# Kernel tuning notes

Measured on AMD Instinct MI355X. Metric: run time of the kernel, lower is better.

The kernel has to match this reference:

```python
import jax, jax.numpy as jnp
import numpy as np

THRESHOLD = 0.5
NEG_POS_RATIO = 3
ALPHA = 1.0


def cxcy_to_xy(c):
    return jnp.concatenate([c[..., :2] - c[..., 2:] / 2, c[..., :2] + c[..., 2:] / 2], axis=-1)


def xy_to_cxcy(x):
    return jnp.concatenate([(x[..., :2] + x[..., 2:]) / 2, x[..., 2:] - x[..., :2]], axis=-1)


def cxcy_to_gcxgcy(cxcy, priors_cxcy):
    return jnp.concatenate([
        (cxcy[..., :2] - priors_cxcy[..., :2]) / (priors_cxcy[..., 2:] / 10.0),
        jnp.log(cxcy[..., 2:] / priors_cxcy[..., 2:]) * 5.0,
    ], axis=-1)


def jaccard(a, b):
    # a: [M,4] xy, b: [P,4] xy -> IoU [M,P]
    lt = jnp.maximum(a[:, None, :2], b[None, :, :2])
    rb = jnp.minimum(a[:, None, 2:], b[None, :, 2:])
    wh = jnp.clip(rb - lt, 0.0)
    inter = wh[..., 0] * wh[..., 1]
    area_a = (a[:, 2] - a[:, 0]) * (a[:, 3] - a[:, 1])
    area_b = (b[:, 2] - b[:, 0]) * (b[:, 3] - b[:, 1])
    return inter / (area_a[:, None] + area_b[None, :] - inter)


def setup_inputs() -> dict:
    key = jax.random.key(0)
    k1, k2, k3, k4, k5, k6, k7 = jax.random.split(key, 7)
    B, P, C, M = 32, 8732, 81, 20
    predicted_locs = jax.random.normal(k1, (B, P, 4), dtype=jnp.float32)
    predicted_scores = jax.random.normal(k2, (B, P, C), dtype=jnp.float32)
    # priors in cxcy format, well inside the unit square
    p_cxy = jax.random.uniform(k3, (P, 2), minval=0.05, maxval=0.95)
    p_wh = jax.random.uniform(k4, (P, 2), minval=0.05, maxval=0.30)
    priors_cxcy = jnp.concatenate([p_cxy, p_wh], axis=-1).astype(jnp.float32)
    # GT boxes: random cxcy -> xy, clipped to [0,1]
    b_cxy = jax.random.uniform(k5, (B, M, 2), minval=0.1, maxval=0.9)
    b_wh = jax.random.uniform(k6, (B, M, 2), minval=0.05, maxval=0.40)
    boxes = jnp.clip(cxcy_to_xy(jnp.concatenate([b_cxy, b_wh], axis=-1)), 0.0, 1.0).astype(jnp.float32)
    labels = jax.random.randint(k7, (B, M), 1, C, dtype=jnp.int64 if jax.config.jax_enable_x64 else jnp.int32)
    return {
        "predicted_locs": predicted_locs,
        "predicted_scores": predicted_scores,
        "boxes": boxes,
        "labels": labels,
        "priors_cxcy": priors_cxcy,
    }


def _match_one(boxes_i, labels_i, priors_cxcy, priors_xy):
    M = boxes_i.shape[0]
    overlap = jaccard(boxes_i, priors_xy)                 # [M, P]
    ov_per_prior = overlap.max(axis=0)                    # [P]
    obj_per_prior = overlap.argmax(axis=0)                # [P]
    prior_per_obj = overlap.argmax(axis=1)                # [M]
    # force-assign each object to its best prior
    obj_per_prior = obj_per_prior.at[prior_per_obj].set(jnp.arange(M))
    ov_per_prior = ov_per_prior.at[prior_per_obj].set(1.0)
    lab = labels_i[obj_per_prior]                         # [P]
    lab = jnp.where(ov_per_prior < THRESHOLD, 0, lab)
    true_locs = cxcy_to_gcxgcy(xy_to_cxcy(boxes_i[obj_per_prior]), priors_cxcy)  # [P,4]
    return true_locs, lab


def reference(predicted_locs, predicted_scores, boxes, labels, priors_cxcy):
    priors_xy = cxcy_to_xy(priors_cxcy)
    true_locs, true_classes = jax.vmap(_match_one, in_axes=(0, 0, None, None))(
        boxes, labels, priors_cxcy, priors_xy)            # [B,P,4], [B,P]

    pos = true_classes > 0                                # [B,P]
    n_pos = pos.sum(axis=1)                               # [B]
    n_pos_total = n_pos.sum().astype(jnp.float32)

    # smooth L1 over positive priors (mean over all selected elements)
    d = predicted_locs - true_locs
    ad = jnp.abs(d)
    sl1 = jnp.where(ad < 1.0, 0.5 * d * d, ad - 0.5)      # [B,P,4]
    loc_loss = jnp.sum(sl1 * pos[..., None]) / (n_pos_total * 4.0)

    # per-prior cross entropy
    logp = jax.nn.log_softmax(predicted_scores, axis=-1)
    ce = -jnp.take_along_axis(logp, true_classes[..., None], axis=-1)[..., 0]  # [B,P]

    conf_pos = jnp.sum(jnp.where(pos, ce, 0.0))
    neg = jnp.where(pos, 0.0, ce)
    neg_sorted = -jnp.sort(-neg, axis=1)                  # descending per image
    ranks = jnp.arange(neg.shape[1])[None, :]
    hard = ranks < (NEG_POS_RATIO * n_pos)[:, None]
    conf_neg = jnp.sum(neg_sorted * hard)

    conf_loss = (conf_neg + conf_pos) / n_pos_total
    return conf_loss, ALPHA * loc_loss
```

## Files before the change

### kernel.cpp

```cpp
#include <hip/hip_runtime.h>
#include <math.h>

#define NB 32
#define NP 8732
#define NC 81
#define NM 20
#define CHUNKS 35
#define NROWS (NB * NP)
#define NGROUPS (NROWS / 4)
#define CE_BLOCKS ((NGROUPS + 63) / 64)
#define MT 1024
#define MV 9

typedef unsigned long long ull;
#define AGENT __HIP_MEMORY_SCOPE_AGENT


__global__ __launch_bounds__(256)
void match_force_kernel(const float* __restrict__ boxes,
                        const int*   __restrict__ labels,
                        const float* __restrict__ priors,
                        ull*      __restrict__ bestpart,
                        unsigned* __restrict__ labobj,
                        int*      __restrict__ chunkdone)
{
    const int b = blockIdx.x / CHUNKS;
    const int chunk = blockIdx.x % CHUNKS;
    const int tid = threadIdx.x;
    const int p = chunk * 256 + tid;
    const bool valid = p < NP;

    __shared__ float bxs[NM][4];
    __shared__ float areaA[NM];
    __shared__ int   labL[NM];
    __shared__ float iouT[256 * 21];
    __shared__ ull   wcand[4][NM];
    __shared__ int   flagLast;
    __shared__ int   pps[NM];

    if (tid < NM * 4) ((float*)bxs)[tid] = boxes[b * NM * 4 + tid];
    if (tid >= 128 && tid < 128 + NM) labL[tid - 128] = labels[b * NM + (tid - 128)];
    if (tid == 0) flagLast = 0;
    __syncthreads();
    if (tid < NM) areaA[tid] = (bxs[tid][2] - bxs[tid][0]) * (bxs[tid][3] - bxs[tid][1]);
    __syncthreads();

    float4 pc = reinterpret_cast<const float4*>(priors)[valid ? p : 0];
    const float px1 = pc.x - pc.z * 0.5f;
    const float py1 = pc.y - pc.w * 0.5f;
    const float px2 = pc.x + pc.z * 0.5f;
    const float py2 = pc.y + pc.w * 0.5f;
    const float pa  = (px2 - px1) * (py2 - py1);

    float bov = -1.f; int bm = 0;
    const int tbase = tid * 21;
#pragma unroll
    for (int m = 0; m < NM; m++) {
        float ix1 = fmaxf(bxs[m][0], px1);
        float iy1 = fmaxf(bxs[m][1], py1);
        float ix2 = fminf(bxs[m][2], px2);
        float iy2 = fminf(bxs[m][3], py2);
        float iw = fmaxf(ix2 - ix1, 0.f);
        float ih = fmaxf(iy2 - iy1, 0.f);
        float inter = iw * ih;
        float iou = inter / (areaA[m] + pa - inter);
        if (iou > bov) { bov = iou; bm = m; }
        iouT[tbase + m] = valid ? iou : -1.f;
    }
    if (valid) {
        int lab = (bov < 0.5f) ? 0 : labL[bm];
        __hip_atomic_store(&labobj[(size_t)b * NP + p],
                           (unsigned)lab | ((unsigned)bm << 8),
                           __ATOMIC_RELAXED, AGENT);
    }
    __syncthreads();

    const int lane = tid & 63, wid = tid >> 6;
    if (lane < NM) {
        const int m = lane;
        float bv = -1.f; int bt = 0;
        const int t0 = wid * 64;
        for (int t = t0; t < t0 + 64; t++) {
            float v = iouT[t * 21 + m];
            if (v > bv) { bv = v; bt = t; }
        }
        wcand[wid][m] = (bv < 0.f) ? 0ull
            : ((((ull)__float_as_uint(bv)) << 32) | (unsigned)~(unsigned)(chunk * 256 + bt));
    }
    __syncthreads();
    if (tid < NM) {
        ull k = wcand[0][tid];
        if (wcand[1][tid] > k) k = wcand[1][tid];
        if (wcand[2][tid] > k) k = wcand[2][tid];
        if (wcand[3][tid] > k) k = wcand[3][tid];
        __hip_atomic_store(&bestpart[(size_t)(b * CHUNKS + chunk) * NM + tid], k,
                           __ATOMIC_RELAXED, AGENT);
    }
    __syncthreads();
    if (tid == 0) {
        int old = __hip_atomic_fetch_add(&chunkdone[b], 1, __ATOMIC_ACQ_REL, AGENT);
        if (old == CHUNKS - 1) flagLast = 1;
    }
    __syncthreads();

    if (flagLast) {
        if (tid < NM) {
            ull k = 0ull;
            for (int c = 0; c < CHUNKS; c++) {
                ull v = __hip_atomic_load(&bestpart[(size_t)(b * CHUNKS + c) * NM + tid],
                                          __ATOMIC_RELAXED, AGENT);
                if (v > k) k = v;
            }
            pps[tid] = (int)~(unsigned)(k & 0xFFFFFFFFull);
        }
        __syncthreads();
        if (tid < NM) {
            int pp = pps[tid];
            bool win = true;
            for (int m2 = tid + 1; m2 < NM; m2++)
                if (pps[m2] == pp) win = false;
            if (win)
                __hip_atomic_store(&labobj[(size_t)b * NP + pp],
                                   (unsigned)labL[tid] | ((unsigned)tid << 8),
                                   __ATOMIC_RELAXED, AGENT);
        }
    }
}

__global__ __launch_bounds__(256)
void ce_kernel(const float* __restrict__ scores,
               const float* __restrict__ plocs,
               const float* __restrict__ boxes,
               const float* __restrict__ priors,
               const unsigned* __restrict__ labobj,
               float* __restrict__ neg,
               float* __restrict__ perimgPos,
               float* __restrict__ perimgLoc,
               int*   __restrict__ nposarr)
{
    __shared__ float bsum, blocsum;
    __shared__ int   bnp[2];
    const int tid = threadIdx.x;
    if (tid == 0) { bsum = 0.f; blocsum = 0.f; }
    if (tid < 2) bnp[tid] = 0;
    __syncthreads();

    const int q = tid & 3;
    const long long g = (long long)blockIdx.x * 64 + (tid >> 2);
    const bool gvalid = g < NGROUPS;
    const float4* gp = reinterpret_cast<const float4*>(scores) + (gvalid ? g : 0) * 81;

    float s0 = 0.f, s1 = 0.f, s2 = 0.f, s3 = 0.f;
#pragma unroll
    for (int j = 0; j < 20; j++) {
        float4 A = gp[q + 4 * j];
        float ex = __expf(A.x), ey = __expf(A.y), ez = __expf(A.z), ew = __expf(A.w);
        if (j <= 4) {
            s0 += (ex + ey) + (ez + ew);
        } else if (j >= 6 && j <= 9) {
            s1 += (ex + ey) + (ez + ew);
        } else if (j >= 11 && j <= 14) {
            s2 += (ex + ey) + (ez + ew);
        } else if (j >= 16) {
            s3 += (ex + ey) + (ez + ew);
        } else {
            const int bnd = (j == 5) ? 81 : (j == 10) ? 162 : 243;
            const int e0 = (q + 4 * j) * 4;
            float lo_ = ((e0     < bnd) ? ex : 0.f) + ((e0 + 1 < bnd) ? ey : 0.f)
                      + ((e0 + 2 < bnd) ? ez : 0.f) + ((e0 + 3 < bnd) ? ew : 0.f);
            float hi_ = ((e0     < bnd) ? 0.f : ex) + ((e0 + 1 < bnd) ? 0.f : ey)
                      + ((e0 + 2 < bnd) ? 0.f : ez) + ((e0 + 3 < bnd) ? 0.f : ew);
            if (j == 5)      { s0 += lo_; s1 += hi_; }
            else if (j == 10){ s1 += lo_; s2 += hi_; }
            else             { s2 += lo_; s3 += hi_; }
        }
    }
    if (q == 0) {
        float4 L = gp[80];
        s3 += (__expf(L.x) + __expf(L.y)) + (__expf(L.z) + __expf(L.w));
    }
    s0 += __shfl_xor(s0, 1);  s0 += __shfl_xor(s0, 2);
    s1 += __shfl_xor(s1, 1);  s1 += __shfl_xor(s1, 2);
    s2 += __shfl_xor(s2, 1);  s2 += __shfl_xor(s2, 2);
    s3 += __shfl_xor(s3, 1);  s3 += __shfl_xor(s3, 2);

    if (gvalid) {
        const float srow = (q == 0) ? s0 : (q == 1) ? s1 : (q == 2) ? s2 : s3;
        const long long r = g * 4 + q;
        const int b = (int)(r / NP);
        const int p = (int)(r - (long long)b * NP);
        const int bfirst = (int)(((long long)blockIdx.x * 256) / NP);
        const unsigned lo = labobj[r];
        const int lab = lo & 0xFF;
        const int obj = lo >> 8;
        float labval = scores[(size_t)r * NC + lab];
        float ce = __logf(srow) - labval;

        if (lab > 0) {
            neg[r] = 0.f;
            atomicAdd(&bsum, ce);
            atomicAdd(&bnp[b - bfirst], 1);
            float4 pcr = reinterpret_cast<const float4*>(priors)[p];
            const float* bx = boxes + ((size_t)b * NM + obj) * 4;
            float x1 = bx[0], y1 = bx[1], x2 = bx[2], y2 = bx[3];
            float bcx = (x1 + x2) * 0.5f, bcy = (y1 + y2) * 0.5f;
            float bw = x2 - x1, bh = y2 - y1;
            float g0 = (bcx - pcr.x) / (pcr.z / 10.f);
            float g1 = (bcy - pcr.y) / (pcr.w / 10.f);
            float g2 = __logf(bw / pcr.z) * 5.f;
            float g3 = __logf(bh / pcr.w) * 5.f;
            float4 pl = reinterpret_cast<const float4*>(plocs)[r];
            float t = 0.f, d, ad;
            d = pl.x - g0; ad = fabsf(d); t += (ad < 1.f) ? 0.5f * d * d : ad - 0.5f;
            d = pl.y - g1; ad = fabsf(d); t += (ad < 1.f) ? 0.5f * d * d : ad - 0.5f;
            d = pl.z - g2; ad = fabsf(d); t += (ad < 1.f) ? 0.5f * d * d : ad - 0.5f;
            d = pl.w - g3; ad = fabsf(d); t += (ad < 1.f) ? 0.5f * d * d : ad - 0.5f;
            atomicAdd(&blocsum, t);
        } else {
            neg[r] = ce;
        }
    }
    __syncthreads();
    if (tid == 0) {
        const int bfirst = (int)(((long long)blockIdx.x * 256) / NP);
        if (bsum != 0.f)    atomicAdd(&perimgPos[bfirst], bsum);
        if (blocsum != 0.f) atomicAdd(&perimgLoc[bfirst], blocsum);
        if (bnp[0] > 0)     atomicAdd(&nposarr[bfirst], bnp[0]);
        if (bnp[1] > 0 && bfirst + 1 < NB) atomicAdd(&nposarr[bfirst + 1], bnp[1]);
    }
}

__global__ __launch_bounds__(MT)
void mine_kernel(const float* __restrict__ neg,
                 const int*   __restrict__ nposarr,
                 const float* __restrict__ perimgPos,
                 const float* __restrict__ perimgLoc,
                 float* __restrict__ acc,
                 float* __restrict__ out)
{
    __shared__ int      hist[2048];
    __shared__ unsigned bres;
    __shared__ int      kkS;
    __shared__ unsigned tbits;
    __shared__ float    redF[MT / 64];
    __shared__ int      redI[MT / 64];

    const int b = blockIdx.x;
    const int tid = threadIdx.x;
    const int lane = tid & 63, wid = tid >> 6;

    float v[MV];
    unsigned mask = 0u;
    const float* src = neg + (size_t)b * NP;
#pragma unroll
    for (int j = 0; j < MV; j++) {
        const int idx = tid + MT * j;
        const bool ok = idx < NP;
        v[j] = ok ? src[idx] : -1.f;
        if (ok) mask |= (1u << j);
    }
    int k = nposarr[b] * 3;
    if (k > NP) k = NP;

    float t = 0.f;
    if (k > 0) {
        float lo = -0.5f;
        float R  = 16.5f;
        if (tid == 0) kkS = k;

        for (int pass = 0; pass < 2; pass++) {
            hist[tid] = 0;
            hist[tid + 1024] = 0;
            __syncthreads();
            const float invw = 2048.f / R;
#pragma unroll
            for (int j = 0; j < MV; j++) {
                if (mask & (1u << j)) {
                    int bin = (int)((v[j] - lo) * invw);
                    bin = (bin < 0) ? 0 : (bin > 2047 ? 2047 : bin);
                    atomicAdd(&hist[bin], 1);
                }
            }
            __syncthreads();
            if (wid == 0) {
                const int kkC = kkS;
                const int base = lane * 32;
                int sL = 0;
#pragma unroll
                for (int i = 0; i < 32; i++) sL += hist[base + i];
                int val = sL;
#pragma unroll
                for (int off = 1; off < 64; off <<= 1) {
                    int tmp = __shfl_down(val, off);
                    if (lane + off < 64) val += tmp;
                }
                const int sufAfter = val - sL;
                if (sufAfter < kkC && kkC <= sufAfter + sL) {
                    int cum = sufAfter;
                    int Bstar = base;
                    int cAbove = sufAfter;
                    for (int i = 31; i >= 0; i--) {
                        const int h = hist[base + i];
                        if (cum + h >= kkC) { Bstar = base + i; cAbove = cum; break; }
                        cum += h;
                    }
                    bres = (unsigned)Bstar;
                    kkS = kkC - cAbove;
                }
            }
            __syncthreads();
            const unsigned Bs = bres;
            const float w = R / 2048.f;
#pragma unroll
            for (int j = 0; j < MV; j++) {
                if (mask & (1u << j)) {
                    int bin = (int)((v[j] - lo) * invw);
                    bin = (bin < 0) ? 0 : (bin > 2047 ? 2047 : bin);
                    if (bin != (int)Bs) mask &= ~(1u << j);
                }
            }
            lo += (float)Bs * w;
            R = w;
        }
        if (tid == 0) tbits = 0u;
        __syncthreads();
        unsigned mb = 0u;
#pragma unroll
        for (int j = 0; j < MV; j++)
            if ((mask & (1u << j)) && v[j] >= 0.f) {
                const unsigned bitsj = __float_as_uint(v[j]);
                if (bitsj > mb) mb = bitsj;
            }
#pragma unroll
        for (int off = 32; off; off >>= 1) {
            const unsigned o = __shfl_xor(mb, off);
            if (o > mb) mb = o;
        }
        if (lane == 0) atomicMax(&tbits, mb);
        __syncthreads();
        t = __uint_as_float(tbits);
    }

    float s = 0.f; int cg = 0;
#pragma unroll
    for (int j = 0; j < MV; j++) {
        const float val = v[j];
        if (val > t) { s += val; cg++; }
    }
#pragma unroll
    for (int off = 32; off; off >>= 1) { s += __shfl_down(s, off); cg += __shfl_down(cg, off); }
    if (lane == 0) { redF[wid] = s; redI[wid] = cg; }
    __syncthreads();
    if (tid == 0) {
        float sum = 0.f; int cG = 0;
#pragma unroll
        for (int w = 0; w < MT / 64; w++) { sum += redF[w]; cG += redI[w]; }
        const float contrib = (k > 0) ? (sum + (float)(k - cG) * t) : 0.f;
        atomicAdd(&acc[2], contrib);
        atomicAdd(&acc[1], perimgPos[b]);
        atomicAdd(&acc[0], perimgLoc[b]);
        __threadfence();
        int old = atomicAdd((int*)acc + 3, 1);
        if (old == NB - 1) {
            __threadfence();
            float nt = 0.f;
            for (int i = 0; i < NB; i++) nt += (float)nposarr[i];
            out[0] = (acc[2] + acc[1]) / nt;
            out[1] = acc[0] / (nt * 4.f);
        }
    }
}

extern "C" void kernel_launch(void* const* d_in, const int* in_sizes, int n_in,
                              void* d_out, int out_size, void* d_ws, size_t ws_size,
                              hipStream_t stream)
{
    const float* plocs  = (const float*)d_in[0];
    const float* scores = (const float*)d_in[1];
    const float* boxes  = (const float*)d_in[2];
    const int*   labels = (const int*)d_in[3];
    const float* priors = (const float*)d_in[4];
    float* out = (float*)d_out;

    char* base = (char*)d_ws;
    float*    acc       = (float*)base;
    int*      nposarr   = (int*)(base + 64);
    int*      chunkdone = (int*)(base + 192);
    float*    perimgPos = (float*)(base + 320);
    float*    perimgLoc = (float*)(base + 448);
    ull*      bestpart  = (ull*)(base + 4096);
    unsigned* labobj    = (unsigned*)(base + 196608);
    float*    neg       = (float*)(base + 1314304);

    hipMemsetAsync(d_ws, 0, 4096, stream);
    hipLaunchKernelGGL(match_force_kernel, dim3(NB * CHUNKS), dim3(256), 0, stream,
                       boxes, labels, priors, bestpart, labobj, chunkdone);
    hipLaunchKernelGGL(ce_kernel, dim3(CE_BLOCKS), dim3(256), 0, stream,
                       scores, plocs, boxes, priors, labobj, neg,
                       perimgPos, perimgLoc, nposarr);
    hipLaunchKernelGGL(mine_kernel, dim3(NB), dim3(MT), 0, stream,
                       neg, nposarr, perimgPos, perimgLoc, acc, out);
}
```

Before: 68.47 us.

## Run log-sum-exp over scores concurrently with box matching in one launch

Moves the bandwidth-heavy log-sum-exp over the score tensor out of the CE kernel and into the same grid as the matching kernel. Block ranges are split so LSE blocks and match blocks run side by side, and a light epilogue kernel then reads the stored LSE plus the label logit to form the CE and loc terms. The aim is to hide the latency-bound matching phase behind the streaming score reads. The cost is an extra workspace buffer that is written and read back, plus a separate gather of the label logit.

```diff
diff --git a/kernel.cpp b/kernel.cpp
--- a/kernel.cpp
+++ b/kernel.cpp
@@ -8,7 +8,9 @@
 #define CHUNKS 35
 #define NROWS (NB * NP)
 #define NGROUPS (NROWS / 4)
-#define CE_BLOCKS ((NGROUPS + 63) / 64)
+#define LSE_BLOCKS ((NGROUPS + 63) / 64)
+#define MATCH_BLOCKS (NB * CHUNKS)
+#define EPI_BLOCKS ((NROWS + 255) / 256)
 #define MT 1024
 #define MV 9
 
@@ -17,19 +19,15 @@
 
 
 __global__ __launch_bounds__(256)
-void match_force_kernel(const float* __restrict__ boxes,
-                        const int*   __restrict__ labels,
-                        const float* __restrict__ priors,
-                        ull*      __restrict__ bestpart,
-                        unsigned* __restrict__ labobj,
-                        int*      __restrict__ chunkdone)
+void lse_match_kernel(const float* __restrict__ scores,
+                      float* __restrict__ lse,
+                      const float* __restrict__ boxes,
+                      const int*   __restrict__ labels,
+                      const float* __restrict__ priors,
+                      ull*      __restrict__ bestpart,
+                      unsigned* __restrict__ labobj,
+                      int*      __restrict__ chunkdone)
 {
-    const int b = blockIdx.x / CHUNKS;
-    const int chunk = blockIdx.x % CHUNKS;
-    const int tid = threadIdx.x;
-    const int p = chunk * 256 + tid;
-    const bool valid = p < NP;
-
     __shared__ float bxs[NM][4];
     __shared__ float areaA[NM];
     __shared__ int   labL[NM];
@@ -37,6 +35,61 @@
     __shared__ ull   wcand[4][NM];
     __shared__ int   flagLast;
     __shared__ int   pps[NM];
+
+    const int tid = threadIdx.x;
+
+    if (blockIdx.x < LSE_BLOCKS) {
+        const int q = tid & 3;
+        const long long g = (long long)blockIdx.x * 64 + (tid >> 2);
+        const bool gvalid = g < NGROUPS;
+        const float4* gp = reinterpret_cast<const float4*>(scores) + (gvalid ? g : 0) * 81;
+
+        float s0 = 0.f, s1 = 0.f, s2 = 0.f, s3 = 0.f;
+#pragma unroll
+        for (int j = 0; j < 20; j++) {
+            const float4 A = gp[q + 4 * j];
+            float ex = __expf(A.x), ey = __expf(A.y), ez = __expf(A.z), ew = __expf(A.w);
+            if (j <= 4) {
+                s0 += (ex + ey) + (ez + ew);
+            } else if (j >= 6 && j <= 9) {
+                s1 += (ex + ey) + (ez + ew);
+            } else if (j >= 11 && j <= 14) {
+                s2 += (ex + ey) + (ez + ew);
+            } else if (j >= 16) {
+                s3 += (ex + ey) + (ez + ew);
+            } else {
+                const int bnd = (j == 5) ? 81 : (j == 10) ? 162 : 243;
+                const int e0 = (q + 4 * j) * 4;
+                float lo_ = ((e0     < bnd) ? ex : 0.f) + ((e0 + 1 < bnd) ? ey : 0.f)
+                          + ((e0 + 2 < bnd) ? ez : 0.f) + ((e0 + 3 < bnd) ? ew : 0.f);
+                float hi_ = ((e0     < bnd) ? 0.f : ex) + ((e0 + 1 < bnd) ? 0.f : ey)
+                          + ((e0 + 2 < bnd) ? 0.f : ez) + ((e0 + 3 < bnd) ? 0.f : ew);
+                if (j == 5)      { s0 += lo_; s1 += hi_; }
+                else if (j == 10){ s1 += lo_; s2 += hi_; }
+                else             { s2 += lo_; s3 += hi_; }
+            }
+        }
+        if (q == 0) {
+            const float4 L = gp[80];
+            s3 += (__expf(L.x) + __expf(L.y)) + (__expf(L.z) + __expf(L.w));
+        }
+        s0 += __shfl_xor(s0, 1);  s0 += __shfl_xor(s0, 2);
+        s1 += __shfl_xor(s1, 1);  s1 += __shfl_xor(s1, 2);
+        s2 += __shfl_xor(s2, 1);  s2 += __shfl_xor(s2, 2);
+        s3 += __shfl_xor(s3, 1);  s3 += __shfl_xor(s3, 2);
+
+        if (gvalid) {
+            const float srow = (q == 0) ? s0 : (q == 1) ? s1 : (q == 2) ? s2 : s3;
+            lse[g * 4 + q] = __logf(srow);
+        }
+        return;
+    }
+
+    const int mbid = blockIdx.x - LSE_BLOCKS;
+    const int b = mbid / CHUNKS;
+    const int chunk = mbid % CHUNKS;
+    const int p = chunk * 256 + tid;
+    const bool valid = p < NP;
 
     if (tid < NM * 4) ((float*)bxs)[tid] = boxes[b * NM * 4 + tid];
     if (tid >= 128 && tid < 128 + NM) labL[tid - 128] = labels[b * NM + (tid - 128)];
@@ -128,15 +181,16 @@
 }
 
 __global__ __launch_bounds__(256)
-void ce_kernel(const float* __restrict__ scores,
-               const float* __restrict__ plocs,
-               const float* __restrict__ boxes,
-               const float* __restrict__ priors,
-               const unsigned* __restrict__ labobj,
-               float* __restrict__ neg,
-               float* __restrict__ perimgPos,
-               float* __restrict__ perimgLoc,
-               int*   __restrict__ nposarr)
+void epilogue_kernel(const float* __restrict__ scores,
+                     const float* __restrict__ plocs,
+                     const float* __restrict__ boxes,
+                     const float* __restrict__ priors,
+                     const unsigned* __restrict__ labobj,
+                     const float* __restrict__ lse,
+                     float* __restrict__ neg,
+                     float* __restrict__ perimgPos,
+                     float* __restrict__ perimgLoc,
+                     int*   __restrict__ nposarr)
 {
     __shared__ float bsum, blocsum;
     __shared__ int   bnp[2];
@@ -145,57 +199,20 @@
     if (tid < 2) bnp[tid] = 0;
     __syncthreads();
 
-    const int q = tid & 3;
-    const long long g = (long long)blockIdx.x * 64 + (tid >> 2);
-    const bool gvalid = g < NGROUPS;
-    const float4* gp = reinterpret_cast<const float4*>(scores) + (gvalid ? g : 0) * 81;
-
-    float s0 = 0.f, s1 = 0.f, s2 = 0.f, s3 = 0.f;
-#pragma unroll
-    for (int j = 0; j < 20; j++) {
-        float4 A = gp[q + 4 * j];
-        float ex = __expf(A.x), ey = __expf(A.y), ez = __expf(A.z), ew = __expf(A.w);
-        if (j <= 4) {
-            s0 += (ex + ey) + (ez + ew);
-        } else if (j >= 6 && j <= 9) {
-            s1 += (ex + ey) + (ez + ew);
-        } else if (j >= 11 && j <= 14) {
-            s2 += (ex + ey) + (ez + ew);
-        } else if (j >= 16) {
-            s3 += (ex + ey) + (ez + ew);
-        } else {
-            const int bnd = (j == 5) ? 81 : (j == 10) ? 162 : 243;
-            const int e0 = (q + 4 * j) * 4;
-            float lo_ = ((e0     < bnd) ? ex : 0.f) + ((e0 + 1 < bnd) ? ey : 0.f)
-                      + ((e0 + 2 < bnd) ? ez : 0.f) + ((e0 + 3 < bnd) ? ew : 0.f);
-            float hi_ = ((e0     < bnd) ? 0.f : ex) + ((e0 + 1 < bnd) ? 0.f : ey)
-                      + ((e0 + 2 < bnd) ? 0.f : ez) + ((e0 + 3 < bnd) ? 0.f : ew);
-            if (j == 5)      { s0 += lo_; s1 += hi_; }
-            else if (j == 10){ s1 += lo_; s2 += hi_; }
-            else             { s2 += lo_; s3 += hi_; }
-        }
-    }
-    if (q == 0) {
-        float4 L = gp[80];
-        s3 += (__expf(L.x) + __expf(L.y)) + (__expf(L.z) + __expf(L.w));
-    }
-    s0 += __shfl_xor(s0, 1);  s0 += __shfl_xor(s0, 2);
-    s1 += __shfl_xor(s1, 1);  s1 += __shfl_xor(s1, 2);
-    s2 += __shfl_xor(s2, 1);  s2 += __shfl_xor(s2, 2);
-    s3 += __shfl_xor(s3, 1);  s3 += __shfl_xor(s3, 2);
-
-    if (gvalid) {
-        const float srow = (q == 0) ? s0 : (q == 1) ? s1 : (q == 2) ? s2 : s3;
-        const long long r = g * 4 + q;
-        const int b = (int)(r / NP);
-        const int p = (int)(r - (long long)b * NP);
-        const int bfirst = (int)(((long long)blockIdx.x * 256) / NP);
-        const unsigned lo = labobj[r];
-        const int lab = lo & 0xFF;
-        const int obj = lo >> 8;
-        float labval = scores[(size_t)r * NC + lab];
-        float ce = __logf(srow) - labval;
-
+    const int r = blockIdx.x * 256 + tid;
+    const bool valid = r < NROWS;
+    const int rr = valid ? r : 0;
+    const int b = rr / NP;
+    const int p = rr - b * NP;
+    const int bfirst = (blockIdx.x * 256) / NP;
+
+    const unsigned lo = labobj[rr];
+    const int lab = lo & 0xFF;
+    const int obj = lo >> 8;
+    const float labval = scores[(size_t)rr * NC + lab];
+    const float ce = lse[rr] - labval;
+
+    if (valid) {
         if (lab > 0) {
             neg[r] = 0.f;
             atomicAdd(&bsum, ce);
@@ -209,7 +226,7 @@
             float g1 = (bcy - pcr.y) / (pcr.w / 10.f);
             float g2 = __logf(bw / pcr.z) * 5.f;
             float g3 = __logf(bh / pcr.w) * 5.f;
-            float4 pl = reinterpret_cast<const float4*>(plocs)[r];
+            float4 pl = reinterpret_cast<const float4*>(plocs)[rr];
             float t = 0.f, d, ad;
             d = pl.x - g0; ad = fabsf(d); t += (ad < 1.f) ? 0.5f * d * d : ad - 0.5f;
             d = pl.y - g1; ad = fabsf(d); t += (ad < 1.f) ? 0.5f * d * d : ad - 0.5f;
@@ -222,7 +239,6 @@
     }
     __syncthreads();
     if (tid == 0) {
-        const int bfirst = (int)(((long long)blockIdx.x * 256) / NP);
         if (bsum != 0.f)    atomicAdd(&perimgPos[bfirst], bsum);
         if (blocsum != 0.f) atomicAdd(&perimgLoc[bfirst], blocsum);
         if (bnp[0] > 0)     atomicAdd(&nposarr[bfirst], bnp[0]);
@@ -391,12 +407,13 @@
     ull*      bestpart  = (ull*)(base + 4096);
     unsigned* labobj    = (unsigned*)(base + 196608);
     float*    neg       = (float*)(base + 1314304);
+    float*    lse       = (float*)(base + 2432000);
 
     hipMemsetAsync(d_ws, 0, 4096, stream);
-    hipLaunchKernelGGL(match_force_kernel, dim3(NB * CHUNKS), dim3(256), 0, stream,
-                       boxes, labels, priors, bestpart, labobj, chunkdone);
-    hipLaunchKernelGGL(ce_kernel, dim3(CE_BLOCKS), dim3(256), 0, stream,
-                       scores, plocs, boxes, priors, labobj, neg,
+    hipLaunchKernelGGL(lse_match_kernel, dim3(LSE_BLOCKS + MATCH_BLOCKS), dim3(256), 0, stream,
+                       scores, lse, boxes, labels, priors, bestpart, labobj, chunkdone);
+    hipLaunchKernelGGL(epilogue_kernel, dim3(EPI_BLOCKS), dim3(256), 0, stream,
+                       scores, plocs, boxes, priors, labobj, lse, neg,
                        perimgPos, perimgLoc, nposarr);
     hipLaunchKernelGGL(mine_kernel, dim3(NB), dim3(MT), 0, stream,
                        neg, nposarr, perimgPos, perimgLoc, acc, out);
```

Result: slower. 71.18 us (+4.0%).
